# Kernel tuning notes

Hardware: AMD Instinct MI355X
Metric: run time of the kernel (lower is better)

Reference implementation:

```python
import jax, jax.numpy as jnp
import numpy as np

D = 512      # slot_dim
DP = 128     # pairwise_dim
H = 8        # num_heads
HD = D // H  # head_dim
EPS = 1e-5


def layernorm(x, w, b):
    mu = jnp.mean(x, axis=-1, keepdims=True)
    var = jnp.var(x, axis=-1, keepdims=True)
    return (x - mu) * jax.lax.rsqrt(var + EPS) * w + b


def setup_inputs() -> dict:
    key = jax.random.key(0)
    ks = jax.random.split(key, 12)
    B, K = 4, 512
    s = 0.02
    return {
        "slots": jax.random.normal(ks[0], (B, K, D), jnp.float32),
        "pairwise": jax.random.normal(ks[1], (B, K, K, DP), jnp.float32),
        "ln1_w": jnp.ones((D,), jnp.float32),
        "ln1_b": jnp.zeros((D,), jnp.float32),
        "ln2_w": jnp.ones((D,), jnp.float32),
        "ln2_b": jnp.zeros((D,), jnp.float32),
        "w_qkv": jax.random.normal(ks[2], (D, 3 * D), jnp.float32) * s,
        "edge_w": jax.random.normal(ks[3], (DP, H), jnp.float32) * s,
        "edge_b": jnp.zeros((H,), jnp.float32),
        "out_w": jax.random.normal(ks[4], (D, D), jnp.float32) * s,
        "out_b": jnp.zeros((D,), jnp.float32),
        "ffn_w1": jax.random.normal(ks[5], (D, 4 * D), jnp.float32) * s,
        "ffn_b1": jnp.zeros((4 * D,), jnp.float32),
        "ffn_w2": jax.random.normal(ks[6], (4 * D, D), jnp.float32) * s,
        "ffn_b2": jnp.zeros((D,), jnp.float32),
    }


def reference(slots, pairwise, ln1_w, ln1_b, ln2_w, ln2_b, w_qkv,
              edge_w, edge_b, out_w, out_b, ffn_w1, ffn_b1, ffn_w2, ffn_b2):
    B, K, _ = slots.shape
    x = layernorm(slots, ln1_w, ln1_b)
    qkv = x @ w_qkv                                   # (B,K,3D)
    q, k, v = jnp.split(qkv, 3, axis=-1)
    # (B,K,D) -> (B,H,K,HD)
    split = lambda t: t.reshape(B, K, H, HD).transpose(0, 2, 1, 3)
    q, k, v = split(q), split(k), split(v)
    attn = jnp.einsum('bhqd,bhkd->bhqk', q, k) * (HD ** -0.5)
    edge_bias = jnp.einsum('bqkp,ph->bhqk', pairwise, edge_w) + edge_b[None, :, None, None]
    attn = jax.nn.softmax(attn + edge_bias, axis=-1)
    out = jnp.einsum('bhqk,bhkd->bhqd', attn, v)      # (B,H,K,HD)
    out = out.transpose(0, 2, 1, 3).reshape(B, K, D)
    slots = slots + out @ out_w + out_b
    y = layernorm(slots, ln2_w, ln2_b)
    h = jax.nn.gelu(y @ ffn_w1 + ffn_b1, approximate=False)
    slots = slots + h @ ffn_w2 + ffn_b2
    return slots
```

## Files before the change

### kernel.cpp

```cpp
#include <hip/hip_runtime.h>
#include <hip/hip_bf16.h>

typedef __attribute__((ext_vector_type(8))) short bf16x8;
typedef __attribute__((ext_vector_type(4))) float f32x4;

#define DEV __device__ __forceinline__

DEV float ldf(const float* p){ return *p; }
DEV float ldf(const unsigned short* p){ return __uint_as_float(((unsigned)*p) << 16); }
DEV void stout(float* p, float v){ *p = v; }
DEV void stout(unsigned short* p, float v){
  __hip_bfloat16 h = __float2bfloat16(v);
  *p = *reinterpret_cast<unsigned short*>(&h);
}

__global__ __launch_bounds__(256) void ln_kernel(const float* __restrict__ in,
    const float* __restrict__ w, const float* __restrict__ bb,
    unsigned short* __restrict__ out)
{
  const int row = blockIdx.x;
  const int tid = threadIdx.x;
  const long base = (long)row * 512;
  float v0 = in[base + tid];
  float v1 = in[base + 256 + tid];
  float s = v0 + v1, ss = v0*v0 + v1*v1;
  #pragma unroll
  for (int o = 32; o > 0; o >>= 1){ s += __shfl_down(s, o); ss += __shfl_down(ss, o); }
  __shared__ float rA[4], rB[4];
  const int wid = tid >> 6, lid = tid & 63;
  if (lid == 0){ rA[wid] = s; rB[wid] = ss; }
  __syncthreads();
  s  = rA[0] + rA[1] + rA[2] + rA[3];
  ss = rB[0] + rB[1] + rB[2] + rB[3];
  float mu  = s * (1.f/512.f);
  float var = ss * (1.f/512.f) - mu*mu;
  float r   = rsqrtf(var + 1e-5f);
  stout(&out[base + tid],       (v0 - mu) * r * w[tid]       + bb[tid]);
  stout(&out[base + 256 + tid], (v1 - mu) * r * w[256 + tid] + bb[256 + tid]);
}

template<typename TIN>
__global__ __launch_bounds__(256) void transpose_conv(
    const TIN* __restrict__ in, unsigned short* __restrict__ out,
    int ldin, int ldout, long sIn, long sOut)
{
  __shared__ float t[32][33];
  in  += (long)blockIdx.z * sIn;
  out += (long)blockIdx.z * sOut;
  const int n0 = blockIdx.x*32, k0 = blockIdx.y*32;
  const int c = threadIdx.x & 31, r0 = threadIdx.x >> 5;
  #pragma unroll
  for (int i = 0; i < 4; i++){
    int r = r0 + i*8;
    t[r][c] = ldf(&in[(long)(k0 + r)*ldin + n0 + c]);
  }
  __syncthreads();
  #pragma unroll
  for (int i = 0; i < 4; i++){
    int r = r0 + i*8;
    stout(&out[(long)(n0 + r)*ldout + k0 + c], t[c][r]);
  }
}

template<int MT,int NT,int WGM,int WGN,int WR,int WC,int EPI,typename TOUT,int BDIV>
__global__ __launch_bounds__(256) void mfma_gemm(
    const unsigned short* __restrict__ A, const unsigned short* __restrict__ B,
    TOUT* __restrict__ C,
    int lda, int ldb, int ldc, int Kd,
    long sA, long sA2, long sB, long sB2, long sC, long sC2,
    const float* __restrict__ bias, const float* __restrict__ res)
{
  const int bz = blockIdx.z;
  A += (long)(bz / BDIV) * sA + (long)(bz % BDIV) * sA2;
  B += (long)(bz / BDIV) * sB + (long)(bz % BDIV) * sB2;
  C += (long)(bz / BDIV) * sC + (long)(bz % BDIV) * sC2;
  if (res) res += (long)(bz / BDIV) * sC + (long)(bz % BDIV) * sC2;
  __shared__ unsigned short As[MT][40];
  __shared__ unsigned short Bs[NT][40];
  const int tid  = threadIdx.x;
  const int lane = tid & 63, wv = tid >> 6;
  const int quad = lane >> 4, l16 = lane & 15;
  const int wm = (wv % WGM) * WR * 16;
  const int wn = (wv / WGM) * WC * 16;
  const int m0 = blockIdx.y * MT, n0 = blockIdx.x * NT;
  f32x4 acc[WR][WC] = {};
  for (int k0 = 0; k0 < Kd; k0 += 32){
    #pragma unroll
    for (int it = 0; it < MT*32/(256*8); ++it){
      int idx = (it*256 + tid) * 8;
      int r = idx >> 5, c = idx & 31;
      *(uint4*)&As[r][c] = *(const uint4*)&A[(long)(m0 + r)*lda + k0 + c];
    }
    #pragma unroll
    for (int it = 0; it < NT*32/(256*8); ++it){
      int idx = (it*256 + tid) * 8;
      int r = idx >> 5, c = idx & 31;
      *(uint4*)&Bs[r][c] = *(const uint4*)&B[(long)(n0 + r)*ldb + k0 + c];
    }
    __syncthreads();
    bf16x8 af[WR], bfr[WC];
    #pragma unroll
    for (int i = 0; i < WR; i++) af[i]  = *(const bf16x8*)&As[wm + i*16 + l16][quad*8];
    #pragma unroll
    for (int j = 0; j < WC; j++) bfr[j] = *(const bf16x8*)&Bs[wn + j*16 + l16][quad*8];
    #pragma unroll
    for (int i = 0; i < WR; i++)
      #pragma unroll
      for (int j = 0; j < WC; j++)
        acc[i][j] = __builtin_amdgcn_mfma_f32_16x16x32_bf16(af[i], bfr[j], acc[i][j], 0, 0, 0);
    __syncthreads();
  }
  #pragma unroll
  for (int i = 0; i < WR; i++){
    #pragma unroll
    for (int j = 0; j < WC; j++){
      #pragma unroll
      for (int r = 0; r < 4; r++){
        int m = m0 + wm + i*16 + quad*4 + r;
        int n = n0 + wn + j*16 + l16;
        float v = acc[i][j][r];
        long idx = (long)m * ldc + n;
        if (EPI == 0){ stout(&C[idx], v); }
        else if (EPI == 2){ stout(&C[idx], v + bias[n] + res[idx]); }
        else if (EPI == 3){
          v += bias[n];
          v = 0.5f * v * (1.f + erff(v * 0.70710678118f));
          stout(&C[idx], v);
        }
        else if (EPI == 4){ ((float*)C)[idx] += 0.125f * v; }
      }
    }
  }
}

__global__ __launch_bounds__(256) void softmax_kernel(
    const float* __restrict__ sc, unsigned short* __restrict__ pr)
{
  const long base = (long)blockIdx.x * 512;
  const int tid = threadIdx.x;
  float a = sc[base + tid], b = sc[base + 256 + tid];
  float m = fmaxf(a, b);
  #pragma unroll
  for (int o = 32; o > 0; o >>= 1) m = fmaxf(m, __shfl_xor(m, o));
  __shared__ float rA[4], rB[4];
  const int wid = tid >> 6, lid = tid & 63;
  if (lid == 0) rA[wid] = m;
  __syncthreads();
  m = fmaxf(fmaxf(rA[0], rA[1]), fmaxf(rA[2], rA[3]));
  float ea = __expf(a - m), eb = __expf(b - m);
  float s = ea + eb;
  #pragma unroll
  for (int o = 32; o > 0; o >>= 1) s += __shfl_xor(s, o);
  if (lid == 0) rB[wid] = s;
  __syncthreads();
  s = rB[0] + rB[1] + rB[2] + rB[3];
  float inv = 1.f / s;
  stout(&pr[base + tid],       ea * inv);
  stout(&pr[base + 256 + tid], eb * inv);
}

__global__ __launch_bounds__(256) void edge_bias_kernel(
    const float* __restrict__ pw,
    const float* __restrict__ edge_w,
    const float* __restrict__ edge_b,
    float* __restrict__ scores)
{
  const int tid  = threadIdx.x;
  const int lane = tid & 63;
  const int wid  = tid >> 6;
  const int sub  = lane & 15;
  const int quad = lane >> 4;
  float ew[8][8];
  #pragma unroll
  for (int j = 0; j < 8; j++)
    #pragma unroll
    for (int h = 0; h < 8; h++)
      ew[j][h] = edge_w[(sub*8 + j)*8 + h];
  const int b3 = (sub >> 3) & 1, b2_ = (sub >> 2) & 1, b1 = (sub >> 1) & 1;
  const int myh = b3*4 + b2_*2 + b1;
  const float ebh = edge_b[myh];
  const long total = 1048576;
  for (long base = (long)blockIdx.x * 16; base < total; base += (long)gridDim.x * 16){
    long pair = base + wid*4 + quad;
    const float* src = pw + pair * 128 + sub * 8;
    float4 r0 = *reinterpret_cast<const float4*>(src);
    float4 r1 = *reinterpret_cast<const float4*>(src + 4);
    float x[8] = {r0.x, r0.y, r0.z, r0.w, r1.x, r1.y, r1.z, r1.w};
    float acc[8] = {0,0,0,0,0,0,0,0};
    #pragma unroll
    for (int j = 0; j < 8; j++)
      #pragma unroll
      for (int h = 0; h < 8; h++)
        acc[h] += x[j] * ew[j][h];
    float t[4];
    #pragma unroll
    for (int i = 0; i < 4; i++){
      float send = b3 ? acc[i] : acc[i+4];
      float keep = b3 ? acc[i+4] : acc[i];
      t[i] = keep + __shfl_xor(send, 8);
    }
    float u[2];
    #pragma unroll
    for (int i = 0; i < 2; i++){
      float send = b2_ ? t[i] : t[i+2];
      float keep = b2_ ? t[i+2] : t[i];
      u[i] = keep + __shfl_xor(send, 4);
    }
    float send = b1 ? u[0] : u[1];
    float keep = b1 ? u[1] : u[0];
    float val = keep + __shfl_xor(send, 2);
    val += __shfl_xor(val, 1);
    if ((sub & 1) == 0){
      long b  = pair >> 18;
      long qk = pair & 262143;
      scores[(b*8 + myh) * 262144 + qk] = val + ebh;
    }
  }
}

extern "C" void kernel_launch(void* const* d_in, const int* in_sizes, int n_in,
                              void* d_out, int out_size, void* d_ws, size_t ws_size,
                              hipStream_t stream)
{
  const float* slots    = (const float*)d_in[0];
  const float* pairwise = (const float*)d_in[1];
  const float* ln1_w    = (const float*)d_in[2];
  const float* ln1_b    = (const float*)d_in[3];
  const float* ln2_w    = (const float*)d_in[4];
  const float* ln2_b    = (const float*)d_in[5];
  const float* w_qkv    = (const float*)d_in[6];
  const float* edge_w   = (const float*)d_in[7];
  const float* edge_b   = (const float*)d_in[8];
  const float* out_w    = (const float*)d_in[9];
  const float* out_b    = (const float*)d_in[10];
  const float* ffn_w1   = (const float*)d_in[11];
  const float* ffn_b1   = (const float*)d_in[12];
  const float* ffn_w2   = (const float*)d_in[13];
  const float* ffn_b2   = (const float*)d_in[14];
  float* out = (float*)d_out;

  float* ws      = (float*)d_ws;
  float* scores  = ws;
  float* slots2  = ws + 8388608;
  unsigned short* ub = (unsigned short*)(ws + 9437184);
  unsigned short* x_b    = ub;
  unsigned short* qkv_b  = ub + 1048576;
  unsigned short* probs  = ub + 4194304;
  unsigned short* vt_b   = ub + 12582912;
  unsigned short* attn_b = ub + 13631488;
  unsigned short* y_b    = ub + 14680064;
  unsigned short* h_b    = ub + 15728640;
  unsigned short* wqkvT  = ub + 19922944;
  unsigned short* outwT  = ub + 20709376;
  unsigned short* w1T    = ub + 20971520;
  unsigned short* w2T    = ub + 22020096;

  transpose_conv<float><<<dim3(48,16,1), 256, 0, stream>>>(w_qkv,  wqkvT, 1536, 512, 0, 0);
  transpose_conv<float><<<dim3(16,16,1), 256, 0, stream>>>(out_w,  outwT, 512,  512, 0, 0);
  transpose_conv<float><<<dim3(64,16,1), 256, 0, stream>>>(ffn_w1, w1T,   2048, 512, 0, 0);
  transpose_conv<float><<<dim3(16,64,1), 256, 0, stream>>>(ffn_w2, w2T,   512, 2048, 0, 0);

  ln_kernel<<<2048, 256, 0, stream>>>(slots, ln1_w, ln1_b, x_b);
  mfma_gemm<128,128,2,2,4,4,0,unsigned short,1><<<dim3(12,16,1), 256, 0, stream>>>(
      x_b, wqkvT, qkv_b, 512, 512, 1536, 512,
      0,0,0,0,0,0, nullptr, nullptr);
  edge_bias_kernel<<<8192, 256, 0, stream>>>(pairwise, edge_w, edge_b, scores);
  mfma_gemm<128,128,2,2,4,4,4,float,8><<<dim3(4,4,32), 256, 0, stream>>>(
      qkv_b, qkv_b + 512, scores, 1536, 1536, 512, 64,
      786432, 64, 786432, 64, 2097152, 262144, nullptr, nullptr);
  softmax_kernel<<<16384, 256, 0, stream>>>(scores, probs);
  transpose_conv<unsigned short><<<dim3(16,16,4), 256, 0, stream>>>(
      qkv_b + 1024, vt_b, 1536, 512, 786432, 262144);
  mfma_gemm<128,64,4,1,2,4,0,unsigned short,8><<<dim3(1,4,32), 256, 0, stream>>>(
      probs, vt_b, attn_b, 512, 512, 512, 512,
      2097152, 262144, 262144, 32768, 262144, 64, nullptr, nullptr);
  mfma_gemm<64,128,1,4,4,2,2,float,1><<<dim3(4,32,1), 256, 0, stream>>>(
      attn_b, outwT, slots2, 512, 512, 512, 512,
      0,0,0,0,0,0, out_b, slots);
  ln_kernel<<<2048, 256, 0, stream>>>(slots2, ln2_w, ln2_b, y_b);
  mfma_gemm<128,128,2,2,4,4,3,unsigned short,1><<<dim3(16,16,1), 256, 0, stream>>>(
      y_b, w1T, h_b, 512, 512, 2048, 512,
      0,0,0,0,0,0, ffn_b1, nullptr);
  mfma_gemm<64,128,1,4,4,2,2,float,1><<<dim3(4,32,1), 256, 0, stream>>>(
      h_b, w2T, out, 2048, 2048, 512, 2048,
      0,0,0,0,0,0, ffn_b2, slots2);
}
```

Baseline: 910.8 us.

## Fuse QK^T, softmax and PV into a flash-style attention kernel

Replaces the separate score GEMM (which accumulated into the edge-bias buffer), the softmax kernel and the PV GEMM with one kernel. It computes QK^T with MFMA, adds the precomputed edge bias, keeps an online softmax, and multiplies by V tile by tile. This removes the round trips of the fp32 score matrix and the bf16 probability matrix through global memory, and two launches. The trade-off is a fixed tiling of 64 queries per block over 256 blocks, plus serial K tiles without prefetch, which may limit occupancy and latency hiding.

New measurement: 862.4 us. 5.3% less time.

```diff
diff --git a/kernel.cpp b/kernel.cpp
--- a/kernel.cpp
+++ b/kernel.cpp
@@ -12,6 +12,10 @@
 DEV void stout(unsigned short* p, float v){
   __hip_bfloat16 h = __float2bfloat16(v);
   *p = *reinterpret_cast<unsigned short*>(&h);
+}
+DEV unsigned short bf16bits(float v){
+  __hip_bfloat16 h = __float2bfloat16(v);
+  return *reinterpret_cast<unsigned short*>(&h);
 }
 
 __global__ __launch_bounds__(256) void ln_kernel(const float* __restrict__ in,
@@ -127,36 +131,9 @@
           v = 0.5f * v * (1.f + erff(v * 0.70710678118f));
           stout(&C[idx], v);
         }
-        else if (EPI == 4){ ((float*)C)[idx] += 0.125f * v; }
       }
     }
   }
-}
-
-__global__ __launch_bounds__(256) void softmax_kernel(
-    const float* __restrict__ sc, unsigned short* __restrict__ pr)
-{
-  const long base = (long)blockIdx.x * 512;
-  const int tid = threadIdx.x;
-  float a = sc[base + tid], b = sc[base + 256 + tid];
-  float m = fmaxf(a, b);
-  #pragma unroll
-  for (int o = 32; o > 0; o >>= 1) m = fmaxf(m, __shfl_xor(m, o));
-  __shared__ float rA[4], rB[4];
-  const int wid = tid >> 6, lid = tid & 63;
-  if (lid == 0) rA[wid] = m;
-  __syncthreads();
-  m = fmaxf(fmaxf(rA[0], rA[1]), fmaxf(rA[2], rA[3]));
-  float ea = __expf(a - m), eb = __expf(b - m);
-  float s = ea + eb;
-  #pragma unroll
-  for (int o = 32; o > 0; o >>= 1) s += __shfl_xor(s, o);
-  if (lid == 0) rB[wid] = s;
-  __syncthreads();
-  s = rB[0] + rB[1] + rB[2] + rB[3];
-  float inv = 1.f / s;
-  stout(&pr[base + tid],       ea * inv);
-  stout(&pr[base + 256 + tid], eb * inv);
 }
 
 __global__ __launch_bounds__(256) void edge_bias_kernel(
@@ -215,6 +192,117 @@
       long qk = pair & 262143;
       scores[(b*8 + myh) * 262144 + qk] = val + ebh;
     }
+  }
+}
+
+__global__ __launch_bounds__(256) void fused_attn(
+    const unsigned short* __restrict__ qkv,
+    const float* __restrict__ bias,
+    const unsigned short* __restrict__ vt,
+    unsigned short* __restrict__ attn_out)
+{
+  __shared__ unsigned short Qs[64][72];
+  __shared__ unsigned short Ks[128][72];
+  __shared__ unsigned short Vs[64][136];
+  __shared__ unsigned short Ps[64][136];
+  const int q0 = blockIdx.x * 64;
+  const int h  = blockIdx.y;
+  const int b  = blockIdx.z;
+  const int tid  = threadIdx.x;
+  const int lane = tid & 63, w = tid >> 6;
+  const int l16  = lane & 15, quad = lane >> 4;
+
+  const unsigned short* Qg = qkv + (long)(b*512 + q0)*1536 + h*64;
+  const unsigned short* Kg = qkv + (long)(b*512)*1536 + 512 + h*64;
+  const unsigned short* Vg = vt  + (long)b*262144 + (long)(h*64)*512;
+  const float*          Bg = bias + ((long)(b*8 + h)*512 + q0)*512;
+
+  #pragma unroll
+  for (int it = 0; it < 2; ++it){
+    int idx = (it*256 + tid)*8; int r = idx >> 6, c = idx & 63;
+    *(uint4*)&Qs[r][c] = *(const uint4*)&Qg[(long)r*1536 + c];
+  }
+  __syncthreads();
+  bf16x8 aq[2];
+  aq[0] = *(const bf16x8*)&Qs[w*16 + l16][quad*8];
+  aq[1] = *(const bf16x8*)&Qs[w*16 + l16][32 + quad*8];
+
+  float m_run[4] = {-1e30f, -1e30f, -1e30f, -1e30f};
+  float l_run[4] = {0.f, 0.f, 0.f, 0.f};
+  f32x4 on[4] = {};
+
+  for (int kt = 0; kt < 4; ++kt){
+    const int k0 = kt * 128;
+    __syncthreads();
+    #pragma unroll
+    for (int it = 0; it < 4; ++it){
+      int idx = (it*256 + tid)*8; int r = idx >> 6, c = idx & 63;
+      *(uint4*)&Ks[r][c] = *(const uint4*)&Kg[(long)(k0 + r)*1536 + c];
+    }
+    #pragma unroll
+    for (int it = 0; it < 4; ++it){
+      int idx = (it*256 + tid)*8; int r = idx >> 7, c = idx & 127;
+      *(uint4*)&Vs[r][c] = *(const uint4*)&Vg[(long)r*512 + k0 + c];
+    }
+    float bb[4][8];
+    #pragma unroll
+    for (int r = 0; r < 4; ++r){
+      const float* bp = Bg + (long)(w*16 + quad*4 + r)*512 + k0 + l16;
+      #pragma unroll
+      for (int j = 0; j < 8; ++j) bb[r][j] = bp[16*j];
+    }
+    __syncthreads();
+    f32x4 sacc[8] = {};
+    #pragma unroll
+    for (int j = 0; j < 8; ++j){
+      bf16x8 bk0 = *(const bf16x8*)&Ks[j*16 + l16][quad*8];
+      bf16x8 bk1 = *(const bf16x8*)&Ks[j*16 + l16][32 + quad*8];
+      sacc[j] = __builtin_amdgcn_mfma_f32_16x16x32_bf16(aq[0], bk0, sacc[j], 0, 0, 0);
+      sacc[j] = __builtin_amdgcn_mfma_f32_16x16x32_bf16(aq[1], bk1, sacc[j], 0, 0, 0);
+    }
+    #pragma unroll
+    for (int r = 0; r < 4; ++r){
+      float s[8];
+      #pragma unroll
+      for (int j = 0; j < 8; ++j) s[j] = fmaf(sacc[j][r], 0.125f, bb[r][j]);
+      float tm = s[0];
+      #pragma unroll
+      for (int j = 1; j < 8; ++j) tm = fmaxf(tm, s[j]);
+      #pragma unroll
+      for (int o = 1; o < 16; o <<= 1) tm = fmaxf(tm, __shfl_xor(tm, o));
+      float mnew  = fmaxf(m_run[r], tm);
+      float alpha = __expf(m_run[r] - mnew);
+      m_run[r] = mnew;
+      float ps = 0.f;
+      #pragma unroll
+      for (int j = 0; j < 8; ++j){
+        float p = __expf(s[j] - mnew);
+        ps += p;
+        Ps[w*16 + quad*4 + r][l16 + 16*j] = bf16bits(p);
+      }
+      #pragma unroll
+      for (int o = 1; o < 16; o <<= 1) ps += __shfl_xor(ps, o);
+      l_run[r] = l_run[r] * alpha + ps;
+      #pragma unroll
+      for (int n = 0; n < 4; ++n) on[n][r] *= alpha;
+    }
+    #pragma unroll
+    for (int ks = 0; ks < 4; ++ks){
+      bf16x8 pa = *(const bf16x8*)&Ps[w*16 + l16][ks*32 + quad*8];
+      #pragma unroll
+      for (int n = 0; n < 4; ++n){
+        bf16x8 bv = *(const bf16x8*)&Vs[n*16 + l16][ks*32 + quad*8];
+        on[n] = __builtin_amdgcn_mfma_f32_16x16x32_bf16(pa, bv, on[n], 0, 0, 0);
+      }
+    }
+  }
+  unsigned short* Og = attn_out + (long)(b*512 + q0)*512 + h*64;
+  #pragma unroll
+  for (int r = 0; r < 4; ++r){
+    float inv = 1.f / l_run[r];
+    #pragma unroll
+    for (int n = 0; n < 4; ++n)
+      Og[(long)(w*16 + quad*4 + r)*512 + n*16 + l16] = bf16bits(on[n][r] * inv);
   }
 }
 
@@ -245,7 +333,6 @@
   unsigned short* ub = (unsigned short*)(ws + 9437184);
   unsigned short* x_b    = ub;
   unsigned short* qkv_b  = ub + 1048576;
-  unsigned short* probs  = ub + 4194304;
   unsigned short* vt_b   = ub + 12582912;
   unsigned short* attn_b = ub + 13631488;
   unsigned short* y_b    = ub + 14680064;
@@ -265,15 +352,9 @@
       x_b, wqkvT, qkv_b, 512, 512, 1536, 512,
       0,0,0,0,0,0, nullptr, nullptr);
   edge_bias_kernel<<<8192, 256, 0, stream>>>(pairwise, edge_w, edge_b, scores);
-  mfma_gemm<128,128,2,2,4,4,4,float,8><<<dim3(4,4,32), 256, 0, stream>>>(
-      qkv_b, qkv_b + 512, scores, 1536, 1536, 512, 64,
-      786432, 64, 786432, 64, 2097152, 262144, nullptr, nullptr);
-  softmax_kernel<<<16384, 256, 0, stream>>>(scores, probs);
   transpose_conv<unsigned short><<<dim3(16,16,4), 256, 0, stream>>>(
       qkv_b + 1024, vt_b, 1536, 512, 786432, 262144);
-  mfma_gemm<128,64,4,1,2,4,0,unsigned short,8><<<dim3(1,4,32), 256, 0, stream>>>(
-      probs, vt_b, attn_b, 512, 512, 512, 512,
-      2097152, 262144, 262144, 32768, 262144, 64, nullptr, nullptr);
+  fused_attn<<<dim3(8,8,4), 256, 0, stream>>>(qkv_b, scores, vt_b, attn_b);
   mfma_gemm<64,128,1,4,4,2,2,float,1><<<dim3(4,32,1), 256, 0, stream>>>(
       attn_b, outwT, slots2, 512, 512, 512, 512,
       0,0,0,0,0,0, out_b, slots);
```
